# Kernel tuning notes

Hardware: AMD Instinct MI355X
Metric: run time of the kernel (lower is better)

The kernel has to match this reference:

```python
import jax
import jax.numpy as jnp
from jax import lax
import numpy as np

NUM_LABELS = 128
PAD, BOS, EOS = 0, 1, 2
B, T = 512, 512
NEG = -10000.0


def setup_inputs() -> dict:
    key = jax.random.key(0)
    k1, k2, k3, k4 = jax.random.split(key, 4)
    features = jax.random.normal(k1, (B, T, NUM_LABELS), dtype=jnp.float32)
    tag_seqs = jax.random.randint(k2, (B, T), 0, NUM_LABELS, dtype=jnp.int32)
    # prefix-valid mask with variable lengths in [T//2, T]
    lengths = jax.random.randint(k3, (B,), T // 2, T + 1, dtype=jnp.int32)
    mask = jnp.arange(T, dtype=jnp.int32)[None, :] < lengths[:, None]
    # transitions: randn then the constrained rows/cols from CRF.__init__
    tr = jax.random.normal(k4, (NUM_LABELS, NUM_LABELS), dtype=jnp.float32)
    tr = tr.at[:, BOS].set(NEG)
    tr = tr.at[EOS, :].set(NEG)
    tr = tr.at[PAD, :].set(NEG)
    tr = tr.at[:, PAD].set(NEG)
    tr = tr.at[PAD, PAD].set(0.0)
    tr = tr.at[PAD, EOS].set(0.0)
    return {"features": features, "tag_seqs": tag_seqs, "mask": mask, "transitions": tr}


def _crf_nll(features, transitions, tag_seqs, mask):
    maskf = mask.astype(features.dtype)  # [B,T]
    # ---- gold path score (score_sentences), fully vectorized over time ----
    emis = jnp.take_along_axis(features, tag_seqs[..., None], axis=-1)[..., 0]  # [B,T]
    trans_steps = transitions[tag_seqs[:, :-1], tag_seqs[:, 1:]]               # [B,T-1]
    gold = emis[:, 0] + transitions[BOS, tag_seqs[:, 0]]
    gold = gold + jnp.sum(maskf[:, 1:] * (emis[:, 1:] + trans_steps), axis=1)
    vlen = jnp.sum(mask.astype(jnp.int32), axis=1) - 1                          # [B]
    last_lab = jnp.take_along_axis(tag_seqs, vlen[:, None], axis=1)[:, 0]
    gold = gold + transitions[last_lab, EOS]
    # ---- log-partition (forward_alg): sequential scan over time ----
    init = transitions[BOS, :][None, :] + features[:, 0]  # [B,L]

    def step(fv, xs):
        feat_t, m_t = xs  # [B,L], [B] bool
        # scores[b, prev, cur] = fv[b,prev] + trans[prev,cur] + emit[b,cur]
        scores = fv[:, :, None] + transitions[None, :, :] + feat_t[:, None, :]
        new_fv = jax.nn.logsumexp(scores, axis=1)  # [B,L]
        fv = jnp.where(m_t[:, None], new_fv, fv)
        return fv, None

    xs = (jnp.swapaxes(features[:, 1:], 0, 1), jnp.swapaxes(mask[:, 1:], 0, 1))
    fv, _ = lax.scan(step, init, xs)
    logZ = jax.nn.logsumexp(fv + transitions[:, EOS][None, :], axis=-1)  # [B]
    return -jnp.mean(gold - logZ)


def reference(features, tag_seqs, mask, transitions):
    return _crf_nll(features, transitions, tag_seqs, mask)
```

## Files before the change

kernel.cpp:

```cpp
#include <hip/hip_runtime.h>
#include <cstdint>
#include <cstddef>

#define NLAB 128
#define TT   512
#define BB   512
#define PAD_ 0
#define BOS_ 1
#define EOS_ 2

typedef float v2f __attribute__((ext_vector_type(2)));

__device__ __forceinline__ bool mask_is_i32(const unsigned char* m8) {
    return m8[1] == 0;
}
__device__ __forceinline__ bool mask_at(const unsigned char* m8, int idx, bool isi) {
    if (isi) return ((const int*)m8)[idx] != 0;
    return m8[idx] != 0;
}

__global__ __launch_bounds__(NLAB) void crf_forward(
        const float* __restrict__ feats,
        const int*   __restrict__ tags,
        const unsigned char* __restrict__ m8,
        const float* __restrict__ tr,
        float* __restrict__ gold_out,
        float* __restrict__ logZ_out) {
    const int b = blockIdx.x;
    const int j = threadIdx.x;
    const bool isi = mask_is_i32(m8);

    __shared__ __align__(16) float p_sh[2][NLAB];
    __shared__ float u3_sh[2];
    __shared__ float red[2], red2[2];
    __shared__ float gsh[2];
    __shared__ int   csh[2];

    const size_t fbase = (size_t)b * TT * NLAB;

    float gpart = 0.f;
    int   cnt   = 0;
    #pragma unroll
    for (int tt = j; tt < TT; tt += NLAB) {
        const int idx = b * TT + tt;
        const bool mm = mask_at(m8, idx, isi);
        cnt += mm ? 1 : 0;
        const int tag = tags[idx];
        if (tt == 0) {
            gpart += feats[fbase + tag] + tr[BOS_ * NLAB + tag];
        } else if (mm) {
            gpart += feats[fbase + (size_t)tt * NLAB + tag]
                   + tr[tags[idx - 1] * NLAB + tag];
        }
    }
    #pragma unroll
    for (int off = 32; off > 0; off >>= 1) {
        gpart += __shfl_down(gpart, off, 64);
        cnt   += __shfl_down(cnt,   off, 64);
    }
    if ((j & 63) == 0) { gsh[j >> 6] = gpart; csh[j >> 6] = cnt; }

    v2f Ecol2[NLAB / 2];
    #pragma unroll
    for (int k2 = 0; k2 < NLAB / 2; ++k2) {
        float e0 = __expf(tr[(2 * k2 + 0) * NLAB + j]);
        float e1 = __expf(tr[(2 * k2 + 1) * NLAB + j]);
        asm volatile("" : "+v"(e0), "+v"(e1));
        v2f e; e.x = e0; e.y = e1;
        Ecol2[k2] = e;
    }

    float u = tr[BOS_ * NLAB + j] + feats[fbase + j];
    if (j == 3) u3_sh[0] = u;
    __syncthreads();

    const int len = csh[0] + csh[1];
    if (j == 0) {
        const int last = tags[b * TT + (len - 1)];
        gold_out[b] = gsh[0] + gsh[1] + tr[last * NLAB + EOS_];
    }

    float norm = u3_sh[0];
    float C = 0.f;
    float feat_next  = feats[fbase + 1 * NLAB + j];
    float feat_next2 = feats[fbase + 2 * NLAB + j];

    for (int t = 1; t < len; ++t) {
        const float p = __expf(u - norm);
        C += norm;
        p_sh[t & 1][j] = p;
        const float ft = feat_next;
        feat_next = feat_next2;
        const int tpre = (t + 2 < len) ? (t + 2) : (len - 1);
        feat_next2 = feats[fbase + (size_t)tpre * NLAB + j];
        __syncthreads();
        const float nn = u3_sh[(t - 1) & 1];

        v2f acc0 = {0.f, 0.f}, acc1 = {0.f, 0.f}, acc2 = {0.f, 0.f}, acc3 = {0.f, 0.f};
        const float4* p4 = (const float4*)p_sh[t & 1];
        #pragma unroll
        for (int k4 = 0; k4 < NLAB / 4; ++k4) {
            const float4 pv = p4[k4];
            v2f plo; plo.x = pv.x; plo.y = pv.y;
            v2f phi; phi.x = pv.z; phi.y = pv.w;
            if (k4 & 1) {
                acc2 = __builtin_elementwise_fma(plo, Ecol2[2 * k4 + 0], acc2);
                acc3 = __builtin_elementwise_fma(phi, Ecol2[2 * k4 + 1], acc3);
            } else {
                acc0 = __builtin_elementwise_fma(plo, Ecol2[2 * k4 + 0], acc0);
                acc1 = __builtin_elementwise_fma(phi, Ecol2[2 * k4 + 1], acc1);
            }
        }
        const v2f accs = (acc0 + acc1) + (acc2 + acc3);
        const float s = accs.x + accs.y;

        u = __logf(s) + ft;
        if (j == 3) u3_sh[t & 1] = u;
        norm = nn;
    }

    const float v = u + tr[j * NLAB + EOS_];
    float m = v;
    #pragma unroll
    for (int off = 32; off > 0; off >>= 1)
        m = fmaxf(m, __shfl_xor(m, off, 64));
    if ((j & 63) == 0) red[j >> 6] = m;
    __syncthreads();
    m = fmaxf(red[0], red[1]);
    float e = __expf(v - m);
    #pragma unroll
    for (int off = 32; off > 0; off >>= 1)
        e += __shfl_xor(e, off, 64);
    if ((j & 63) == 0) red2[j >> 6] = e;
    __syncthreads();
    if (j == 0) logZ_out[b] = C + m + __logf(red2[0] + red2[1]);
}

__global__ void crf_finalize(const float* __restrict__ gold,
                             const float* __restrict__ logZ,
                             float* __restrict__ out) {
    __shared__ float sh[4];
    const int i = threadIdx.x;
    float v = (logZ[i] - gold[i]) + (logZ[i + 256] - gold[i + 256]);
    #pragma unroll
    for (int off = 32; off > 0; off >>= 1)
        v += __shfl_xor(v, off, 64);
    if ((i & 63) == 0) sh[i >> 6] = v;
    __syncthreads();
    if (i == 0) out[0] = (sh[0] + sh[1] + sh[2] + sh[3]) * (1.0f / (float)BB);
}

extern "C" void kernel_launch(void* const* d_in, const int* in_sizes, int n_in,
                              void* d_out, int out_size, void* d_ws, size_t ws_size,
                              hipStream_t stream) {
    const float*         feats = (const float*)d_in[0];
    const int*           tags  = (const int*)d_in[1];
    const unsigned char* m8    = (const unsigned char*)d_in[2];
    const float*         tr    = (const float*)d_in[3];

    float* gold = (float*)d_ws;
    float* logZ = gold + BB;
    float* out  = (float*)d_out;

    hipLaunchKernelGGL(crf_forward,  dim3(BB), dim3(NLAB), 0, stream,
                       feats, tags, m8, tr, gold, logZ);
    hipLaunchKernelGGL(crf_finalize, dim3(1),  dim3(256),  0, stream,
                       gold, logZ, out);
}
```

Baseline: 476.3 us.

## Batch 16 sequences per block and compute CRF forward recurrence with bf16 MFMA

```diff
diff --git a/kernel.cpp b/kernel.cpp
--- a/kernel.cpp
+++ b/kernel.cpp
@@ -5,11 +5,13 @@
 #define NLAB 128
 #define TT   512
 #define BB   512
+#define MB   16
 #define PAD_ 0
 #define BOS_ 1
 #define EOS_ 2
 
-typedef float v2f __attribute__((ext_vector_type(2)));
+typedef float f32x4 __attribute__((ext_vector_type(4)));
+typedef short s16x8 __attribute__((ext_vector_type(8)));
 
 __device__ __forceinline__ bool mask_is_i32(const unsigned char* m8) {
     return m8[1] == 0;
@@ -19,121 +21,231 @@
     return m8[idx] != 0;
 }
 
-__global__ __launch_bounds__(NLAB) void crf_forward(
+__device__ __forceinline__ unsigned short f2bf(float f) {
+    union { float f; unsigned u; } v; v.f = f;
+    unsigned r = v.u + 0x7FFFu + ((v.u >> 16) & 1u);
+    return (unsigned short)(r >> 16);
+}
+
+__device__ __forceinline__ s16x8 ebfrag(const float* __restrict__ tr, int kbase, int n) {
+    s16x8 r;
+    #pragma unroll
+    for (int jj = 0; jj < 8; ++jj)
+        r[jj] = (short)f2bf(__expf(tr[(kbase + jj) * NLAB + n]));
+    return r;
+}
+
+__global__ __launch_bounds__(512, 2) void crf_forward(
         const float* __restrict__ feats,
         const int*   __restrict__ tags,
         const unsigned char* __restrict__ m8,
         const float* __restrict__ tr,
         float* __restrict__ gold_out,
         float* __restrict__ logZ_out) {
-    const int b = blockIdx.x;
-    const int j = threadIdx.x;
+    const int tid  = threadIdx.x;
+    const int blk  = blockIdx.x;
+    const int w    = tid >> 6;
+    const int l    = tid & 63;
+    const int quad = l >> 4;
+    const int col  = l & 15;
+    const int j    = w * 16 + col;
     const bool isi = mask_is_i32(m8);
 
-    __shared__ __align__(16) float p_sh[2][NLAB];
-    __shared__ float u3_sh[2];
-    __shared__ float red[2], red2[2];
-    __shared__ float gsh[2];
-    __shared__ int   csh[2];
-
-    const size_t fbase = (size_t)b * TT * NLAB;
-
-    float gpart = 0.f;
-    int   cnt   = 0;
-    #pragma unroll
-    for (int tt = j; tt < TT; tt += NLAB) {
-        const int idx = b * TT + tt;
-        const bool mm = mask_at(m8, idx, isi);
-        cnt += mm ? 1 : 0;
-        const int tag = tags[idx];
-        if (tt == 0) {
-            gpart += feats[fbase + tag] + tr[BOS_ * NLAB + tag];
-        } else if (mm) {
-            gpart += feats[fbase + (size_t)tt * NLAB + tag]
-                   + tr[tags[idx - 1] * NLAB + tag];
+    __shared__ unsigned short P16[2][2048];
+    __shared__ float u3_sh[2][MB];
+    __shared__ float gsh[MB];
+    __shared__ int   csh[MB];
+    __shared__ int   len_sh[MB];
+    __shared__ float red_m[8][MB];
+    __shared__ float red_s[8][MB];
+    __shared__ float mfin[MB];
+
+    {
+        const int bl = tid >> 5, sub = tid & 31;
+        const int Bg = blk * MB + bl;
+        const size_t fb = (size_t)Bg * TT * NLAB;
+        float gp = 0.f; int cnt = 0;
+        for (int tt = sub; tt < TT; tt += 32) {
+            const int idx = Bg * TT + tt;
+            const bool mm = mask_at(m8, idx, isi);
+            cnt += mm ? 1 : 0;
+            const int tg = tags[idx];
+            if (tt == 0) gp += feats[fb + tg] + tr[BOS_ * NLAB + tg];
+            else if (mm) gp += feats[fb + (size_t)tt * NLAB + tg]
+                             + tr[tags[idx - 1] * NLAB + tg];
         }
-    }
-    #pragma unroll
-    for (int off = 32; off > 0; off >>= 1) {
-        gpart += __shfl_down(gpart, off, 64);
-        cnt   += __shfl_down(cnt,   off, 64);
-    }
-    if ((j & 63) == 0) { gsh[j >> 6] = gpart; csh[j >> 6] = cnt; }
-
-    v2f Ecol2[NLAB / 2];
-    #pragma unroll
-    for (int k2 = 0; k2 < NLAB / 2; ++k2) {
-        float e0 = __expf(tr[(2 * k2 + 0) * NLAB + j]);
-        float e1 = __expf(tr[(2 * k2 + 1) * NLAB + j]);
-        asm volatile("" : "+v"(e0), "+v"(e1));
-        v2f e; e.x = e0; e.y = e1;
-        Ecol2[k2] = e;
-    }
-
-    float u = tr[BOS_ * NLAB + j] + feats[fbase + j];
-    if (j == 3) u3_sh[0] = u;
-    __syncthreads();
-
-    const int len = csh[0] + csh[1];
-    if (j == 0) {
-        const int last = tags[b * TT + (len - 1)];
-        gold_out[b] = gsh[0] + gsh[1] + tr[last * NLAB + EOS_];
-    }
-
-    float norm = u3_sh[0];
-    float C = 0.f;
-    float feat_next  = feats[fbase + 1 * NLAB + j];
-    float feat_next2 = feats[fbase + 2 * NLAB + j];
-
-    for (int t = 1; t < len; ++t) {
-        const float p = __expf(u - norm);
-        C += norm;
-        p_sh[t & 1][j] = p;
-        const float ft = feat_next;
-        feat_next = feat_next2;
-        const int tpre = (t + 2 < len) ? (t + 2) : (len - 1);
-        feat_next2 = feats[fbase + (size_t)tpre * NLAB + j];
+        #pragma unroll
+        for (int off = 16; off > 0; off >>= 1) {
+            gp  += __shfl_xor(gp,  off, 64);
+            cnt += __shfl_xor(cnt, off, 64);
+        }
+        if (sub == 0) { gsh[bl] = gp; csh[bl] = cnt; }
+    }
+    __syncthreads();
+    if (tid < MB) {
+        const int len = csh[tid];
+        len_sh[tid] = len;
+        const int Bg = blk * MB + tid;
+        const int last = tags[Bg * TT + (len - 1)];
+        gold_out[Bg] = gsh[tid] + tr[last * NLAB + EOS_];
+    }
+
+    const s16x8 Bf0 = ebfrag(tr, 0 * 32 + quad * 8, j);
+    const s16x8 Bf1 = ebfrag(tr, 1 * 32 + quad * 8, j);
+    const s16x8 Bf2 = ebfrag(tr, 2 * 32 + quad * 8, j);
+    const s16x8 Bf3 = ebfrag(tr, 3 * 32 + quad * 8, j);
+
+    const float trB = tr[BOS_ * NLAB + j];
+    const float trE = tr[j * NLAB + EOS_];
+
+    const int fb0 = (blk * MB + quad * 4 + 0) * (TT * NLAB) + j;
+    const int fb1 = (blk * MB + quad * 4 + 1) * (TT * NLAB) + j;
+    const int fb2 = (blk * MB + quad * 4 + 2) * (TT * NLAB) + j;
+    const int fb3 = (blk * MB + quad * 4 + 3) * (TT * NLAB) + j;
+
+    float u0 = trB + feats[fb0];
+    float u1 = trB + feats[fb1];
+    float u2 = trB + feats[fb2];
+    float u3r = trB + feats[fb3];
+    if (w == 0 && col == 3) {
+        u3_sh[0][quad * 4 + 0] = u0;
+        u3_sh[0][quad * 4 + 1] = u1;
+        u3_sh[0][quad * 4 + 2] = u2;
+        u3_sh[0][quad * 4 + 3] = u3r;
+    }
+    __syncthreads();
+
+    const int4 L4 = ((const int4*)len_sh)[quad];
+    const int len0 = L4.x, len1 = L4.y, len2 = L4.z, len3 = L4.w;
+    int maxlen = 0;
+    #pragma unroll
+    for (int b = 0; b < MB; ++b) maxlen = max(maxlen, len_sh[b]);
+
+    float4 n4 = ((const float4*)u3_sh[0])[quad];
+    float C0 = 0.f, C1 = 0.f, C2 = 0.f, C3 = 0.f;
+
+    const int wa0 = ((j >> 3) * 16 + quad * 4 + 0) * 8 + (j & 7);
+    const int wa1 = wa0 + 8, wa2 = wa0 + 16, wa3 = wa0 + 24;
+    const int ca0 = ((0 * 4 + quad) * 16 + col);
+    const int ca1 = ((1 * 4 + quad) * 16 + col);
+    const int ca2 = ((2 * 4 + quad) * 16 + col);
+    const int ca3 = ((3 * 4 + quad) * 16 + col);
+
+    float fA0 = feats[fb0 + 1 * NLAB], fA1 = feats[fb1 + 1 * NLAB],
+          fA2 = feats[fb2 + 1 * NLAB], fA3 = feats[fb3 + 1 * NLAB];
+    float fB0 = feats[fb0 + 2 * NLAB], fB1 = feats[fb1 + 2 * NLAB],
+          fB2 = feats[fb2 + 2 * NLAB], fB3 = feats[fb3 + 2 * NLAB];
+    float fC0 = feats[fb0 + 3 * NLAB], fC1 = feats[fb1 + 3 * NLAB],
+          fC2 = feats[fb2 + 3 * NLAB], fC3 = feats[fb3 + 3 * NLAB];
+    float fD0 = feats[fb0 + 4 * NLAB], fD1 = feats[fb1 + 4 * NLAB],
+          fD2 = feats[fb2 + 4 * NLAB], fD3 = feats[fb3 + 4 * NLAB];
+
+    for (int t = 1; t < maxlen; ++t) {
+        const bool lv0 = t < len0, lv1 = t < len1, lv2 = t < len2, lv3 = t < len3;
+        const float p0 = __expf(u0 - n4.x);
+        const float p1 = __expf(u1 - n4.y);
+        const float p2 = __expf(u2 - n4.z);
+        const float p3 = __expf(u3r - n4.w);
+        if (lv0) C0 += n4.x;
+        if (lv1) C1 += n4.y;
+        if (lv2) C2 += n4.z;
+        if (lv3) C3 += n4.w;
+
+        const int buf = t & 1;
+        unsigned short* Pb = P16[buf];
+        Pb[wa0] = f2bf(p0);
+        Pb[wa1] = f2bf(p1);
+        Pb[wa2] = f2bf(p2);
+        Pb[wa3] = f2bf(p3);
+
+        const float ft0 = fA0, ft1 = fA1, ft2 = fA2, ft3 = fA3;
+        fA0 = fB0; fA1 = fB1; fA2 = fB2; fA3 = fB3;
+        fB0 = fC0; fB1 = fC1; fB2 = fC2; fB3 = fC3;
+        fC0 = fD0; fC1 = fD1; fC2 = fD2; fC3 = fD3;
+        int tp = t + 4; if (tp >= maxlen) tp = maxlen - 1;
+        const int fo = tp * NLAB;
+        fD0 = feats[fb0 + fo]; fD1 = feats[fb1 + fo];
+        fD2 = feats[fb2 + fo]; fD3 = feats[fb3 + fo];
+
         __syncthreads();
-        const float nn = u3_sh[(t - 1) & 1];
-
-        v2f acc0 = {0.f, 0.f}, acc1 = {0.f, 0.f}, acc2 = {0.f, 0.f}, acc3 = {0.f, 0.f};
-        const float4* p4 = (const float4*)p_sh[t & 1];
+        const float4 nn4 = ((const float4*)u3_sh[(t - 1) & 1])[quad];
+
+        const s16x8* PA = (const s16x8*)Pb;
+        const s16x8 a0 = PA[ca0];
+        const s16x8 a1 = PA[ca1];
+        const s16x8 a2 = PA[ca2];
+        const s16x8 a3 = PA[ca3];
+        f32x4 acc = {0.f, 0.f, 0.f, 0.f};
+        acc = __builtin_amdgcn_mfma_f32_16x16x32_bf16(a0, Bf0, acc, 0, 0, 0);
+        acc = __builtin_amdgcn_mfma_f32_16x16x32_bf16(a1, Bf1, acc, 0, 0, 0);
+        acc = __builtin_amdgcn_mfma_f32_16x16x32_bf16(a2, Bf2, acc, 0, 0, 0);
+        acc = __builtin_amdgcn_mfma_f32_16x16x32_bf16(a3, Bf3, acc, 0, 0, 0);
+
+        if (lv0) u0 = __logf(acc[0]) + ft0;
+        if (lv1) u1 = __logf(acc[1]) + ft1;
+        if (lv2) u2 = __logf(acc[2]) + ft2;
+        if (lv3) u3r = __logf(acc[3]) + ft3;
+
+        if (w == 0 && col == 3) {
+            u3_sh[buf][quad * 4 + 0] = u0;
+            u3_sh[buf][quad * 4 + 1] = u1;
+            u3_sh[buf][quad * 4 + 2] = u2;
+            u3_sh[buf][quad * 4 + 3] = u3r;
+        }
+        n4 = nn4;
+    }
+
+    float v0 = u0 + C0 + trE;
+    float v1 = u1 + C1 + trE;
+    float v2 = u2 + C2 + trE;
+    float v3 = u3r + C3 + trE;
+    float m0 = v0, m1 = v1, m2 = v2, m3 = v3;
+    #pragma unroll
+    for (int off = 1; off < 16; off <<= 1) {
+        m0 = fmaxf(m0, __shfl_xor(m0, off, 64));
+        m1 = fmaxf(m1, __shfl_xor(m1, off, 64));
+        m2 = fmaxf(m2, __shfl_xor(m2, off, 64));
+        m3 = fmaxf(m3, __shfl_xor(m3, off, 64));
+    }
+    if (col == 0) {
+        red_m[w][quad * 4 + 0] = m0;
+        red_m[w][quad * 4 + 1] = m1;
+        red_m[w][quad * 4 + 2] = m2;
+        red_m[w][quad * 4 + 3] = m3;
+    }
+    __syncthreads();
+    if (tid < MB) {
+        float mm = red_m[0][tid];
         #pragma unroll
-        for (int k4 = 0; k4 < NLAB / 4; ++k4) {
-            const float4 pv = p4[k4];
-            v2f plo; plo.x = pv.x; plo.y = pv.y;
-            v2f phi; phi.x = pv.z; phi.y = pv.w;
-            if (k4 & 1) {
-                acc2 = __builtin_elementwise_fma(plo, Ecol2[2 * k4 + 0], acc2);
-                acc3 = __builtin_elementwise_fma(phi, Ecol2[2 * k4 + 1], acc3);
-            } else {
-                acc0 = __builtin_elementwise_fma(plo, Ecol2[2 * k4 + 0], acc0);
-                acc1 = __builtin_elementwise_fma(phi, Ecol2[2 * k4 + 1], acc1);
-            }
-        }
-        const v2f accs = (acc0 + acc1) + (acc2 + acc3);
-        const float s = accs.x + accs.y;
-
-        u = __logf(s) + ft;
-        if (j == 3) u3_sh[t & 1] = u;
-        norm = nn;
-    }
-
-    const float v = u + tr[j * NLAB + EOS_];
-    float m = v;
-    #pragma unroll
-    for (int off = 32; off > 0; off >>= 1)
-        m = fmaxf(m, __shfl_xor(m, off, 64));
-    if ((j & 63) == 0) red[j >> 6] = m;
-    __syncthreads();
-    m = fmaxf(red[0], red[1]);
-    float e = __expf(v - m);
-    #pragma unroll
-    for (int off = 32; off > 0; off >>= 1)
-        e += __shfl_xor(e, off, 64);
-    if ((j & 63) == 0) red2[j >> 6] = e;
-    __syncthreads();
-    if (j == 0) logZ_out[b] = C + m + __logf(red2[0] + red2[1]);
+        for (int ww = 1; ww < 8; ++ww) mm = fmaxf(mm, red_m[ww][tid]);
+        mfin[tid] = mm;
+    }
+    __syncthreads();
+    const float4 M4 = ((const float4*)mfin)[quad];
+    float e0 = __expf(v0 - M4.x);
+    float e1 = __expf(v1 - M4.y);
+    float e2 = __expf(v2 - M4.z);
+    float e3 = __expf(v3 - M4.w);
+    #pragma unroll
+    for (int off = 1; off < 16; off <<= 1) {
+        e0 += __shfl_xor(e0, off, 64);
+        e1 += __shfl_xor(e1, off, 64);
+        e2 += __shfl_xor(e2, off, 64);
+        e3 += __shfl_xor(e3, off, 64);
+    }
+    if (col == 0) {
+        red_s[w][quad * 4 + 0] = e0;
+        red_s[w][quad * 4 + 1] = e1;
+        red_s[w][quad * 4 + 2] = e2;
+        red_s[w][quad * 4 + 3] = e3;
+    }
+    __syncthreads();
+    if (tid < MB) {
+        float ss = 0.f;
+        #pragma unroll
+        for (int ww = 0; ww < 8; ++ww) ss += red_s[ww][tid];
+        logZ_out[blk * MB + tid] = mfin[tid] + __logf(ss);
+    }
 }
 
 __global__ void crf_finalize(const float* __restrict__ gold,
@@ -162,8 +274,8 @@
     float* logZ = gold + BB;
     float* out  = (float*)d_out;
 
-    hipLaunchKernelGGL(crf_forward,  dim3(BB), dim3(NLAB), 0, stream,
+    hipLaunchKernelGGL(crf_forward,  dim3(BB / MB), dim3(512), 0, stream,
                        feats, tags, m8, tr, gold, logZ);
-    hipLaunchKernelGGL(crf_finalize, dim3(1),  dim3(256),  0, stream,
+    hipLaunchKernelGGL(crf_finalize, dim3(1), dim3(256), 0, stream,
                        gold, logZ, out);
 }
```

After: 537.2 us. 12.8% more time.

## Batch 16 sequences per block and run CRF forward recursion on bf16 MFMA

Applied to the files above, without the earlier changes.

```diff
diff --git a/kernel.cpp b/kernel.cpp
--- a/kernel.cpp
+++ b/kernel.cpp
@@ -5,11 +5,14 @@
 #define NLAB 128
 #define TT   512
 #define BB   512
+#define MB   16
 #define PAD_ 0
 #define BOS_ 1
 #define EOS_ 2
-
-typedef float v2f __attribute__((ext_vector_type(2)));
+#define LN2F 0.6931471805599453f
+
+typedef float f32x4 __attribute__((ext_vector_type(4)));
+typedef short s16x8 __attribute__((ext_vector_type(8)));
 
 __device__ __forceinline__ bool mask_is_i32(const unsigned char* m8) {
     return m8[1] == 0;
@@ -19,121 +22,191 @@
     return m8[idx] != 0;
 }
 
-__global__ __launch_bounds__(NLAB) void crf_forward(
+__device__ __forceinline__ unsigned f2bf(float f) {
+    union { float f; unsigned u; } v; v.f = f;
+    return (v.u + 0x7FFFu + ((v.u >> 16) & 1u)) >> 16;
+}
+
+__device__ __forceinline__ s16x8 eafrag(const float* __restrict__ tr, int kbase, int m) {
+    s16x8 r;
+    #pragma unroll
+    for (int jj = 0; jj < 8; ++jj)
+        r[jj] = (short)f2bf(__expf(tr[(kbase + jj) * NLAB + m]));
+    return r;
+}
+
+__global__ __launch_bounds__(512, 2) void crf_forward(
         const float* __restrict__ feats,
         const int*   __restrict__ tags,
         const unsigned char* __restrict__ m8,
         const float* __restrict__ tr,
         float* __restrict__ gold_out,
         float* __restrict__ logZ_out) {
-    const int b = blockIdx.x;
-    const int j = threadIdx.x;
+    const int tid  = threadIdx.x;
+    const int blk  = blockIdx.x;
+    const int w    = tid >> 6;
+    const int l    = tid & 63;
+    const int quad = l >> 4;
+    const int col  = l & 15;
     const bool isi = mask_is_i32(m8);
 
-    __shared__ __align__(16) float p_sh[2][NLAB];
-    __shared__ float u3_sh[2];
-    __shared__ float red[2], red2[2];
-    __shared__ float gsh[2];
-    __shared__ int   csh[2];
-
-    const size_t fbase = (size_t)b * TT * NLAB;
-
-    float gpart = 0.f;
-    int   cnt   = 0;
+    __shared__ __align__(16) unsigned short P16[2][2048];
+    __shared__ int   scale_sh[2][MB];
+    __shared__ float n_sh[MB];
+    __shared__ float gsh[MB];
+    __shared__ int   csh[MB];
+    __shared__ int   len_sh[MB];
+    __shared__ float red_s[8][MB];
+
+    {
+        const int bl = tid >> 5, sub = tid & 31;
+        const int Bg = blk * MB + bl;
+        const size_t fb = (size_t)Bg * TT * NLAB;
+        float gp = 0.f; int cnt = 0;
+        for (int tt = sub; tt < TT; tt += 32) {
+            const int idx = Bg * TT + tt;
+            const bool mm = mask_at(m8, idx, isi);
+            cnt += mm ? 1 : 0;
+            const int tg = tags[idx];
+            if (tt == 0) gp += feats[fb + tg] + tr[BOS_ * NLAB + tg];
+            else if (mm) gp += feats[fb + (size_t)tt * NLAB + tg]
+                             + tr[tags[idx - 1] * NLAB + tg];
+        }
+        #pragma unroll
+        for (int off = 16; off > 0; off >>= 1) {
+            gp  += __shfl_xor(gp,  off, 64);
+            cnt += __shfl_xor(cnt, off, 64);
+        }
+        if (sub == 0) { gsh[bl] = gp; csh[bl] = cnt; }
+    }
+    __syncthreads();
+    if (tid < MB) {
+        const int len = csh[tid];
+        len_sh[tid] = len;
+        const int Bg = blk * MB + tid;
+        const int last = tags[Bg * TT + (len - 1)];
+        gold_out[Bg] = gsh[tid] + tr[last * NLAB + EOS_];
+        scale_sh[0][tid] = 0;
+    }
+
+    const int m_abs = w * 16 + col;
+    const s16x8 Af0 = eafrag(tr, 0 * 32 + quad * 8, m_abs);
+    const s16x8 Af1 = eafrag(tr, 1 * 32 + quad * 8, m_abs);
+    const s16x8 Af2 = eafrag(tr, 2 * 32 + quad * 8, m_abs);
+    const s16x8 Af3 = eafrag(tr, 3 * 32 + quad * 8, m_abs);
+
+    const int mlab0 = w * 16 + quad * 4;
+    const float trB0 = tr[BOS_ * NLAB + mlab0 + 0];
+    const float trB1 = tr[BOS_ * NLAB + mlab0 + 1];
+    const float trB2 = tr[BOS_ * NLAB + mlab0 + 2];
+    const float trB3 = tr[BOS_ * NLAB + mlab0 + 3];
+    const float trE0 = tr[(mlab0 + 0) * NLAB + EOS_];
+    const float trE1 = tr[(mlab0 + 1) * NLAB + EOS_];
+    const float trE2 = tr[(mlab0 + 2) * NLAB + EOS_];
+    const float trE3 = tr[(mlab0 + 3) * NLAB + EOS_];
+
+    const int Bg = blk * MB + col;
+    const size_t fcol = (size_t)Bg * TT * NLAB + mlab0;
+
+    const float4 f0 = *(const float4*)(feats + fcol);
+    const float u0 = trB0 + f0.x, u1 = trB1 + f0.y,
+                u2 = trB2 + f0.z, u3 = trB3 + f0.w;
+    if (w == 0 && quad == 0) n_sh[col] = u3;
+    __syncthreads();
+
+    const int mylen = len_sh[col];
+    int maxlen = 0;
     #pragma unroll
-    for (int tt = j; tt < TT; tt += NLAB) {
-        const int idx = b * TT + tt;
-        const bool mm = mask_at(m8, idx, isi);
-        cnt += mm ? 1 : 0;
-        const int tag = tags[idx];
-        if (tt == 0) {
-            gpart += feats[fbase + tag] + tr[BOS_ * NLAB + tag];
-        } else if (mm) {
-            gpart += feats[fbase + (size_t)tt * NLAB + tag]
-                   + tr[tags[idx - 1] * NLAB + tag];
+    for (int b = 0; b < MB; ++b) maxlen = max(maxlen, len_sh[b]);
+    const float n0 = n_sh[col];
+
+    float4 pf;
+    pf.x = __expf(u0 - n0); pf.y = __expf(u1 - n0);
+    pf.z = __expf(u2 - n0); pf.w = __expf(u3 - n0);
+    float C = n0;
+
+    const int wbase = ((w * 2 + (quad >> 1)) * 16 + col) * 8 + (quad & 1) * 4;
+    {
+        const unsigned lo = f2bf(pf.x) | (f2bf(pf.y) << 16);
+        const unsigned hi = f2bf(pf.z) | (f2bf(pf.w) << 16);
+        *(uint2*)(&P16[0][wbase]) = make_uint2(lo, hi);
+    }
+
+#define LDF(tt) (*(const float4*)(feats + fcol + (size_t)(tt) * NLAB))
+    float4 fA = LDF(min(1, maxlen - 1)), fB = LDF(min(2, maxlen - 1)),
+           fC = LDF(min(3, maxlen - 1)), fD = LDF(min(4, maxlen - 1)),
+           fE = LDF(min(5, maxlen - 1)), fF = LDF(min(6, maxlen - 1)),
+           fG = LDF(min(7, maxlen - 1)), fH = LDF(min(8, maxlen - 1));
+
+    const f32x4 zacc = {0.f, 0.f, 0.f, 0.f};
+    const s16x8* PA0 = (const s16x8*)P16[0];
+    const s16x8* PA1 = (const s16x8*)P16[1];
+    const int ra0 = (0 * 4 + quad) * 16 + col;
+    const int ra1 = (1 * 4 + quad) * 16 + col;
+    const int ra2 = (2 * 4 + quad) * 16 + col;
+    const int ra3 = (3 * 4 + quad) * 16 + col;
+
+#define STEP(ii, FR) {                                                        \
+        const int t = t0 + (ii);                                              \
+        __syncthreads();                                                      \
+        const int pb = (t - 1) & 1;                                           \
+        const int e  = scale_sh[pb][col];                                     \
+        const s16x8* PA = pb ? PA1 : PA0;                                     \
+        const s16x8 b0 = PA[ra0], b1 = PA[ra1], b2 = PA[ra2], b3 = PA[ra3];   \
+        f32x4 acc0 = __builtin_amdgcn_mfma_f32_16x16x32_bf16(Af0, b0, zacc, 0, 0, 0); \
+        acc0 = __builtin_amdgcn_mfma_f32_16x16x32_bf16(Af1, b1, acc0, 0, 0, 0);       \
+        f32x4 acc1 = __builtin_amdgcn_mfma_f32_16x16x32_bf16(Af2, b2, zacc, 0, 0, 0); \
+        acc1 = __builtin_amdgcn_mfma_f32_16x16x32_bf16(Af3, b3, acc1, 0, 0, 0);       \
+        const f32x4 acc = acc0 + acc1;                                        \
+        const bool live = t < mylen;                                          \
+        const float qx = ldexpf(acc[0] * __expf(FR.x), -e);                   \
+        const float qy = ldexpf(acc[1] * __expf(FR.y), -e);                   \
+        const float qz = ldexpf(acc[2] * __expf(FR.z), -e);                   \
+        const float qw = ldexpf(acc[3] * __expf(FR.w), -e);                   \
+        if (live) { pf.x = qx; pf.y = qy; pf.z = qz; pf.w = qw;               \
+                    C += (float)e * LN2F; }                                   \
+        const unsigned lo = f2bf(pf.x) | (f2bf(pf.y) << 16);                  \
+        const unsigned hi = f2bf(pf.z) | (f2bf(pf.w) << 16);                  \
+        *(uint2*)(&P16[t & 1][wbase]) = make_uint2(lo, hi);                   \
+        if (w == 0 && quad == 0) {                                            \
+            const int se = (int)((__float_as_uint(pf.w) >> 23) & 255u) - 126; \
+            scale_sh[t & 1][col] = se;                                        \
+        }                                                                     \
+    }
+
+    for (int t0 = 1; t0 < maxlen; t0 += 8) {
+        const int nstep = min(8, maxlen - t0);
+        if (nstep > 0) STEP(0, fA)
+        if (nstep > 1) STEP(1, fB)
+        if (nstep > 2) STEP(2, fC)
+        if (nstep > 3) STEP(3, fD)
+        if (nstep > 4) STEP(4, fE)
+        if (nstep > 5) STEP(5, fF)
+        if (nstep > 6) STEP(6, fG)
+        if (nstep > 7) STEP(7, fH)
+        if (t0 + 8 < maxlen) {
+            const int mx = maxlen - 1;
+            fA = LDF(min(t0 + 8,  mx)); fB = LDF(min(t0 + 9,  mx));
+            fC = LDF(min(t0 + 10, mx)); fD = LDF(min(t0 + 11, mx));
+            fE = LDF(min(t0 + 12, mx)); fF = LDF(min(t0 + 13, mx));
+            fG = LDF(min(t0 + 14, mx)); fH = LDF(min(t0 + 15, mx));
         }
     }
-    #pragma unroll
-    for (int off = 32; off > 0; off >>= 1) {
-        gpart += __shfl_down(gpart, off, 64);
-        cnt   += __shfl_down(cnt,   off, 64);
-    }
-    if ((j & 63) == 0) { gsh[j >> 6] = gpart; csh[j >> 6] = cnt; }
-
-    v2f Ecol2[NLAB / 2];
-    #pragma unroll
-    for (int k2 = 0; k2 < NLAB / 2; ++k2) {
-        float e0 = __expf(tr[(2 * k2 + 0) * NLAB + j]);
-        float e1 = __expf(tr[(2 * k2 + 1) * NLAB + j]);
-        asm volatile("" : "+v"(e0), "+v"(e1));
-        v2f e; e.x = e0; e.y = e1;
-        Ecol2[k2] = e;
-    }
-
-    float u = tr[BOS_ * NLAB + j] + feats[fbase + j];
-    if (j == 3) u3_sh[0] = u;
-    __syncthreads();
-
-    const int len = csh[0] + csh[1];
-    if (j == 0) {
-        const int last = tags[b * TT + (len - 1)];
-        gold_out[b] = gsh[0] + gsh[1] + tr[last * NLAB + EOS_];
-    }
-
-    float norm = u3_sh[0];
-    float C = 0.f;
-    float feat_next  = feats[fbase + 1 * NLAB + j];
-    float feat_next2 = feats[fbase + 2 * NLAB + j];
-
-    for (int t = 1; t < len; ++t) {
-        const float p = __expf(u - norm);
-        C += norm;
-        p_sh[t & 1][j] = p;
-        const float ft = feat_next;
-        feat_next = feat_next2;
-        const int tpre = (t + 2 < len) ? (t + 2) : (len - 1);
-        feat_next2 = feats[fbase + (size_t)tpre * NLAB + j];
-        __syncthreads();
-        const float nn = u3_sh[(t - 1) & 1];
-
-        v2f acc0 = {0.f, 0.f}, acc1 = {0.f, 0.f}, acc2 = {0.f, 0.f}, acc3 = {0.f, 0.f};
-        const float4* p4 = (const float4*)p_sh[t & 1];
+#undef STEP
+#undef LDF
+
+    float s = pf.x * __expf(trE0) + pf.y * __expf(trE1)
+            + pf.z * __expf(trE2) + pf.w * __expf(trE3);
+    s += __shfl_xor(s, 16, 64);
+    s += __shfl_xor(s, 32, 64);
+    if (l < 16) red_s[w][col] = s;
+    __syncthreads();
+    if (tid < MB) {
+        float S = 0.f;
         #pragma unroll
-        for (int k4 = 0; k4 < NLAB / 4; ++k4) {
-            const float4 pv = p4[k4];
-            v2f plo; plo.x = pv.x; plo.y = pv.y;
-            v2f phi; phi.x = pv.z; phi.y = pv.w;
-            if (k4 & 1) {
-                acc2 = __builtin_elementwise_fma(plo, Ecol2[2 * k4 + 0], acc2);
-                acc3 = __builtin_elementwise_fma(phi, Ecol2[2 * k4 + 1], acc3);
-            } else {
-                acc0 = __builtin_elementwise_fma(plo, Ecol2[2 * k4 + 0], acc0);
-                acc1 = __builtin_elementwise_fma(phi, Ecol2[2 * k4 + 1], acc1);
-            }
-        }
-        const v2f accs = (acc0 + acc1) + (acc2 + acc3);
-        const float s = accs.x + accs.y;
-
-        u = __logf(s) + ft;
-        if (j == 3) u3_sh[t & 1] = u;
-        norm = nn;
-    }
-
-    const float v = u + tr[j * NLAB + EOS_];
-    float m = v;
-    #pragma unroll
-    for (int off = 32; off > 0; off >>= 1)
-        m = fmaxf(m, __shfl_xor(m, off, 64));
-    if ((j & 63) == 0) red[j >> 6] = m;
-    __syncthreads();
-    m = fmaxf(red[0], red[1]);
-    float e = __expf(v - m);
-    #pragma unroll
-    for (int off = 32; off > 0; off >>= 1)
-        e += __shfl_xor(e, off, 64);
-    if ((j & 63) == 0) red2[j >> 6] = e;
-    __syncthreads();
-    if (j == 0) logZ_out[b] = C + m + __logf(red2[0] + red2[1]);
+        for (int ww = 0; ww < 8; ++ww) S += red_s[ww][tid];
+        logZ_out[blk * MB + tid] = C + __logf(S);
+    }
 }
 
 __global__ void crf_finalize(const float* __restrict__ gold,
@@ -162,8 +235,8 @@
     float* logZ = gold + BB;
     float* out  = (float*)d_out;
 
-    hipLaunchKernelGGL(crf_forward,  dim3(BB), dim3(NLAB), 0, stream,
+    hipLaunchKernelGGL(crf_forward,  dim3(BB / MB), dim3(512), 0, stream,
                        feats, tags, m8, tr, gold, logZ);
-    hipLaunchKernelGGL(crf_finalize, dim3(1),  dim3(256),  0, stream,
+    hipLaunchKernelGGL(crf_finalize, dim3(1), dim3(256), 0, stream,
                        gold, logZ, out);
 }
```

Measured after the change: 474.5 us. About the same (-0.4%).
